# Performance work log

Hardware: AMD Instinct MI355X
Metric: run time of the kernel (lower is better)

The kernel has to match this reference:

```python
import jax, jax.numpy as jnp
import numpy as np

B, U, D, N, O = 128, 16, 256, 1024, 256
RES_CONN, IN_CONN, BIAS_P = 0.2, 0.2, 0.5


def _fixed_bernoulli(rng, heads, rows, cols, conn):
    # each column has exactly nb = int(conn*rows) ones (as in the torch code)
    nb = max(1, int(conn * rows))
    r = rng.random((heads, rows, cols))
    thr = np.sort(r, axis=1)[:, nb - 1:nb, :]
    return (r <= thr).astype(np.float32)


def setup_inputs() -> dict:
    rng = np.random.default_rng(0)
    # recurrent weights: normal * fixed-bernoulli mask, normalized by spectral radius
    W = rng.normal(size=(U, N, N)).astype(np.float32) * _fixed_bernoulli(rng, U, N, N, RES_CONN)
    sr0 = np.abs(np.linalg.eigvals(W.astype(np.float64))).max(axis=-1).astype(np.float32).reshape(U, 1, 1)
    W = W / sr0
    Win = _fixed_bernoulli(rng, U, D, N, IN_CONN)
    bias = (rng.random((U, 1, N)) < BIAS_P).astype(np.float32)
    Wout = rng.normal(size=(U, N, O)).astype(np.float32)
    adaptive_lr = rng.random((U, D, 1)).astype(np.float32)
    sr = rng.random((U, 1, 1)).astype(np.float32)
    temperature = np.ones((1,), np.float32)
    X = rng.normal(size=(B, U, D)).astype(np.float32)
    state = rng.normal(size=(B, U, N)).astype(np.float32)
    arrs = dict(X=X, state=state, W=W, Win=Win, bias=bias, Wout=Wout,
                sr=sr, adaptive_lr=adaptive_lr, temperature=temperature)
    return {k: jnp.asarray(v) for k, v in arrs.items()}


def reference(X, state, W, Win, bias, Wout, sr, adaptive_lr, temperature):
    # X: [B,U,D] -> [B,U,1,D]; state: [B,U,N] -> [B,U,1,N]
    x = X[:, :, None, :]
    s = state[:, :, None, :]
    # adaptive per-unit learning rate: softmax over the units axis
    lr = jax.nn.softmax(jnp.einsum('buid,udk->buik', x, adaptive_lr) / temperature, axis=1)  # [B,U,1,1]
    feed = jnp.einsum('buid,udn->buin', x, Win)            # [B,U,1,N]
    echo = jnp.einsum('buin,unm->buim', s, W * sr) + bias  # [B,U,1,N]
    new_state = (1.0 - lr) * s + lr * jnp.tanh(feed + echo)
    output = jnp.einsum('buin,uno->buio', new_state, Wout)  # [B,U,1,O]
    return new_state[:, :, 0, :], output[:, :, 0, :]
```

## Files before the change

### kernel.cpp

```cpp
#include <hip/hip_runtime.h>
#include <math.h>

#define Bsz 128
#define Usz 16
#define Dsz 256
#define Nsz 1024
#define Osz 256

typedef __attribute__((ext_vector_type(4))) float f32x4;
typedef __attribute__((ext_vector_type(8))) short bf16x8;

__device__ __forceinline__ unsigned short f2bf(float f) {
    union { float f; unsigned int u; } v; v.f = f;
    unsigned int lsb = (v.u >> 16) & 1u;
    v.u += 0x7fffu + lsb;
    return (unsigned short)(v.u >> 16);
}

__device__ __forceinline__ bf16x8 pack8(const float* x, float s) {
    union { bf16x8 v; unsigned short h[8]; } r;
    #pragma unroll
    for (int i = 0; i < 8; i++) r.h[i] = f2bf(x[i] * s);
    return r.v;
}

__global__ __launch_bounds__(256)
void lr_kernel(const float* __restrict__ X, const float* __restrict__ alr,
               const float* __restrict__ temp, float* __restrict__ lr)
{
    const int b = blockIdx.x;
    const int t = threadIdx.x;
    const int u = t >> 4;
    const int l = t & 15;
    const float* xp = X + ((size_t)b * Usz + u) * Dsz;
    const float* ap = alr + (size_t)u * Dsz;
    float s = 0.f;
    for (int d = l; d < Dsz; d += 16) s += xp[d] * ap[d];
    s += __shfl_down(s, 8, 16);
    s += __shfl_down(s, 4, 16);
    s += __shfl_down(s, 2, 16);
    s += __shfl_down(s, 1, 16);
    __shared__ float logits[16];
    if (l == 0) logits[u] = s;
    __syncthreads();
    if (t < 16) {
        const float T = temp[0];
        float m = -1e30f;
        #pragma unroll
        for (int i = 0; i < 16; i++) m = fmaxf(m, logits[i] / T);
        float sum = 0.f;
        #pragma unroll
        for (int i = 0; i < 16; i++) sum += expf(logits[i] / T - m);
        lr[(size_t)b * Usz + t] = expf(logits[t] / T - m) / sum;
    }
}

__global__ __launch_bounds__(256)
void state_mfma(const float* __restrict__ X, const float* __restrict__ state,
                const float* __restrict__ W, const float* __restrict__ Win,
                const float* __restrict__ bias, const float* __restrict__ sr,
                const float* __restrict__ lr, float* __restrict__ out0)
{
    const int id   = blockIdx.x;
    const int u    = id & 15;
    const int rest = id >> 4;
    const int nt   = rest & 15;
    const int mt   = rest >> 4;

    const int tid  = threadIdx.x;
    const int wave = tid >> 6, lane = tid & 63;
    const int l16  = lane & 15, kgl = lane >> 4;
    const int wrow = (wave & 1) * 16, wcol = (wave >> 1) * 32;

    __shared__ __align__(16) unsigned short As[2][1024];
    __shared__ __align__(16) unsigned short Bs[2][2048];

    f32x4 acc[2] = {};

    const int  sm  = tid & 31;
    const int  skg = (tid >> 5) & 3;
    const bool doA = tid < 128;
    const int  sb_n = tid & 63, sb_kg = tid >> 6;
    const float sru = sr[u];

    const float* Af = X     + ((size_t)(mt * 32 + sm) * Usz + u) * Dsz + skg * 8;
    const float* Ae = state + ((size_t)(mt * 32 + sm) * Usz + u) * Nsz + skg * 8;
    const float* Bf = Win + (size_t)u * Dsz * Nsz + (size_t)(sb_kg * 8) * Nsz + nt * 64 + sb_n;
    const float* Be = W   + (size_t)u * Nsz * Nsz + (size_t)(sb_kg * 8) * Nsz + nt * 64 + sb_n;

    float areg[8], breg[8];
    auto loadA = [&](int kb) {
        if (!doA) return;
        const float* p = (kb < Dsz) ? (Af + kb) : (Ae + (kb - Dsz));
        const f32x4 v0 = *(const f32x4*)p;
        const f32x4 v1 = *(const f32x4*)(p + 4);
        #pragma unroll
        for (int i = 0; i < 4; i++) { areg[i] = v0[i]; areg[4 + i] = v1[i]; }
    };
    auto loadB = [&](int kb) {
        const float* p = (kb < Dsz) ? (Bf + (size_t)kb * Nsz)
                                    : (Be + (size_t)(kb - Dsz) * Nsz);
        #pragma unroll
        for (int j = 0; j < 8; j++) breg[j] = p[(size_t)j * Nsz];
    };

    const int wrA = ((sm >> 4) * 4 + skg) * 128 + (sm & 15) * 8;
    const int wrB = ((sb_n >> 4) * 4 + sb_kg) * 128 + (sb_n & 15) * 8;
    auto writeBuf = [&](int buf, int kb) {
        const float asc = (kb < Dsz) ? 1.f : sru;
        if (doA) *(bf16x8*)&As[buf][wrA] = pack8(areg, asc);
        *(bf16x8*)&Bs[buf][wrB] = pack8(breg, 1.f);
    };

    loadA(0); loadB(0);
    writeBuf(0, 0);
    loadA(32); loadB(32);
    __syncthreads();

    const int aoff  = (((wave & 1) * 4 + kgl) * 16 + l16) * 8;
    const int boff0 = ((((wcol >> 4) + 0) * 4 + kgl) * 16 + l16) * 8;
    const int boff1 = ((((wcol >> 4) + 1) * 4 + kgl) * 16 + l16) * 8;

    for (int step = 0; step < 40; ++step) {
        const int buf = step & 1;
        if (step + 1 < 40) writeBuf(buf ^ 1, (step + 1) * 32);
        if (step + 2 < 40) { loadA((step + 2) * 32); loadB((step + 2) * 32); }
        const bf16x8 afr = *(const bf16x8*)&As[buf][aoff];
        const bf16x8 b0  = *(const bf16x8*)&Bs[buf][boff0];
        const bf16x8 b1  = *(const bf16x8*)&Bs[buf][boff1];
        acc[0] = __builtin_amdgcn_mfma_f32_16x16x32_bf16(afr, b0, acc[0], 0, 0, 0);
        acc[1] = __builtin_amdgcn_mfma_f32_16x16x32_bf16(afr, b1, acc[1], 0, 0, 0);
        __syncthreads();
    }

    #pragma unroll
    for (int ni = 0; ni < 2; ni++) {
        const int gcol = nt * 64 + wcol + ni * 16 + l16;
        const float bi = bias[u * Nsz + gcol];
        #pragma unroll
        for (int rg = 0; rg < 4; rg++) {
            const int grow = mt * 32 + wrow + kgl * 4 + rg;
            const size_t idx = ((size_t)grow * Usz + u) * Nsz + gcol;
            const float th = tanhf(acc[ni][rg] + bi);
            const float sv = state[idx];
            const float lv = lr[grow * Usz + u];
            out0[idx] = (1.f - lv) * sv + lv * th;
        }
    }
}

__global__ __launch_bounds__(256)
void out_mfma(const float* __restrict__ ns, const float* __restrict__ Wout,
              float* __restrict__ out1)
{
    const int id   = blockIdx.x;
    const int u    = id & 15;
    const int rest = id >> 4;
    const int ot   = rest & 3;
    const int mt   = rest >> 2;

    const int tid  = threadIdx.x;
    const int wave = tid >> 6, lane = tid & 63;
    const int l16  = lane & 15, kgl = lane >> 4;
    const int wcol = wave * 16;

    __shared__ __align__(16) unsigned short As[2][512];
    __shared__ __align__(16) unsigned short Bs[2][2048];

    f32x4 acc = {};

    const bool doA = tid < 64;
    const int  sm  = tid & 15, skg = (tid >> 4) & 3;
    const int  sb_n = tid & 63, sb_kg = tid >> 6;

    const float* Ap = ns + ((size_t)(mt * 16 + sm) * Usz + u) * Nsz + skg * 8;
    const float* Bp = Wout + (size_t)u * Nsz * Osz + (size_t)(sb_kg * 8) * Osz + ot * 64 + sb_n;

    float areg[8], breg[8];
    auto loadA = [&](int kb) {
        if (!doA) return;
        const f32x4 v0 = *(const f32x4*)(Ap + kb);
        const f32x4 v1 = *(const f32x4*)(Ap + kb + 4);
        #pragma unroll
        for (int i = 0; i < 4; i++) { areg[i] = v0[i]; areg[4 + i] = v1[i]; }
    };
    auto loadB = [&](int kb) {
        const float* p = Bp + (size_t)kb * Osz;
        #pragma unroll
        for (int j = 0; j < 8; j++) breg[j] = p[(size_t)j * Osz];
    };

    const int wrA = skg * 128 + sm * 8;
    const int wrB = ((sb_n >> 4) * 4 + sb_kg) * 128 + (sb_n & 15) * 8;
    auto writeBuf = [&](int buf) {
        if (doA) *(bf16x8*)&As[buf][wrA] = pack8(areg, 1.f);
        *(bf16x8*)&Bs[buf][wrB] = pack8(breg, 1.f);
    };

    loadA(0); loadB(0);
    writeBuf(0);
    loadA(32); loadB(32);
    __syncthreads();

    const int aoff = (kgl * 16 + l16) * 8;
    const int boff = ((wave * 4 + kgl) * 16 + l16) * 8;

    for (int step = 0; step < 32; ++step) {
        const int buf = step & 1;
        if (step + 1 < 32) writeBuf(buf ^ 1);
        if (step + 2 < 32) { loadA((step + 2) * 32); loadB((step + 2) * 32); }
        const bf16x8 afr = *(const bf16x8*)&As[buf][aoff];
        const bf16x8 bfr = *(const bf16x8*)&Bs[buf][boff];
        acc = __builtin_amdgcn_mfma_f32_16x16x32_bf16(afr, bfr, acc, 0, 0, 0);
        __syncthreads();
    }

    const int gcol = ot * 64 + wcol + l16;
    #pragma unroll
    for (int rg = 0; rg < 4; rg++) {
        const int grow = mt * 16 + kgl * 4 + rg;
        out1[((size_t)grow * Usz + u) * Osz + gcol] = acc[rg];
    }
}

extern "C" void kernel_launch(void* const* d_in, const int* in_sizes, int n_in,
                              void* d_out, int out_size, void* d_ws, size_t ws_size,
                              hipStream_t stream)
{
    (void)in_sizes; (void)n_in; (void)out_size; (void)ws_size;
    const float* X     = (const float*)d_in[0];
    const float* state = (const float*)d_in[1];
    const float* W     = (const float*)d_in[2];
    const float* Win   = (const float*)d_in[3];
    const float* bias  = (const float*)d_in[4];
    const float* Wout  = (const float*)d_in[5];
    const float* sr    = (const float*)d_in[6];
    const float* alr   = (const float*)d_in[7];
    const float* temp  = (const float*)d_in[8];

    float* out0 = (float*)d_out;
    float* out1 = out0 + (size_t)Bsz * Usz * Nsz;
    float* lr   = (float*)d_ws;

    lr_kernel<<<Bsz, 256, 0, stream>>>(X, alr, temp, lr);
    state_mfma<<<1024, 256, 0, stream>>>(X, state, W, Win, bias, sr, lr, out0);
    out_mfma<<<512, 256, 0, stream>>>(out0, Wout, out1);
}
```

Baseline: 203.8 us.

## Use full-batch M tiles, truncating bf16 packs, and split-K output GEMM

```diff
diff --git a/kernel.cpp b/kernel.cpp
--- a/kernel.cpp
+++ b/kernel.cpp
@@ -9,19 +9,21 @@
 
 typedef __attribute__((ext_vector_type(4))) float f32x4;
 typedef __attribute__((ext_vector_type(8))) short bf16x8;
-
-__device__ __forceinline__ unsigned short f2bf(float f) {
-    union { float f; unsigned int u; } v; v.f = f;
-    unsigned int lsb = (v.u >> 16) & 1u;
-    v.u += 0x7fffu + lsb;
-    return (unsigned short)(v.u >> 16);
-}
-
-__device__ __forceinline__ bf16x8 pack8(const float* x, float s) {
-    union { bf16x8 v; unsigned short h[8]; } r;
-    #pragma unroll
-    for (int i = 0; i < 8; i++) r.h[i] = f2bf(x[i] * s);
-    return r.v;
+typedef __attribute__((ext_vector_type(4))) unsigned int u32x4;
+
+union cell_u { u32x4 u; bf16x8 b; };
+
+__device__ __forceinline__ unsigned int fbits(float f) {
+    union { float f; unsigned int u; } v; v.f = f; return v.u;
+}
+__device__ __forceinline__ unsigned int pk(float lo, float hi) {
+    return __builtin_amdgcn_perm(fbits(hi), fbits(lo), 0x07060302u);
+}
+__device__ __forceinline__ u32x4 pk8(const float* x) {
+    u32x4 r;
+    r[0] = pk(x[0], x[1]); r[1] = pk(x[2], x[3]);
+    r[2] = pk(x[4], x[5]); r[3] = pk(x[6], x[7]);
+    return r;
 }
 
 __global__ __launch_bounds__(256)
@@ -61,55 +63,57 @@
                 const float* __restrict__ bias, const float* __restrict__ sr,
                 const float* __restrict__ lr, float* __restrict__ out0)
 {
-    const int id   = blockIdx.x;
-    const int u    = id & 15;
-    const int rest = id >> 4;
-    const int nt   = rest & 15;
-    const int mt   = rest >> 4;
+    const int id = blockIdx.x;
+    const int u  = id & 15;
+    const int nt = id >> 4;
 
     const int tid  = threadIdx.x;
     const int wave = tid >> 6, lane = tid & 63;
     const int l16  = lane & 15, kgl = lane >> 4;
-    const int wrow = (wave & 1) * 16, wcol = (wave >> 1) * 32;
-
-    __shared__ __align__(16) unsigned short As[2][1024];
-    __shared__ __align__(16) unsigned short Bs[2][2048];
-
-    f32x4 acc[2] = {};
-
-    const int  sm  = tid & 31;
-    const int  skg = (tid >> 5) & 3;
-    const bool doA = tid < 128;
-    const int  sb_n = tid & 63, sb_kg = tid >> 6;
+
+    __shared__ u32x4 As[2][512];
+    __shared__ u32x4 Bs[2][256];
+
+    f32x4 acc[8] = {};
+
+    const int am = tid & 127, akg2 = tid >> 7;
+    const int bn = tid & 63,  bkg  = tid >> 6;
     const float sru = sr[u];
 
-    const float* Af = X     + ((size_t)(mt * 32 + sm) * Usz + u) * Dsz + skg * 8;
-    const float* Ae = state + ((size_t)(mt * 32 + sm) * Usz + u) * Nsz + skg * 8;
-    const float* Bf = Win + (size_t)u * Dsz * Nsz + (size_t)(sb_kg * 8) * Nsz + nt * 64 + sb_n;
-    const float* Be = W   + (size_t)u * Nsz * Nsz + (size_t)(sb_kg * 8) * Nsz + nt * 64 + sb_n;
-
-    float areg[8], breg[8];
+    const float* Af = X     + ((size_t)am * Usz + u) * Dsz;
+    const float* Ae = state + ((size_t)am * Usz + u) * Nsz;
+    const float* Bf = Win + (size_t)u * Dsz * Nsz + nt * 64 + bn;
+    const float* Be = W   + (size_t)u * Nsz * Nsz + nt * 64 + bn;
+
+    float ar[16], br[8];
+
     auto loadA = [&](int kb) {
-        if (!doA) return;
-        const float* p = (kb < Dsz) ? (Af + kb) : (Ae + (kb - Dsz));
-        const f32x4 v0 = *(const f32x4*)p;
-        const f32x4 v1 = *(const f32x4*)(p + 4);
-        #pragma unroll
-        for (int i = 0; i < 4; i++) { areg[i] = v0[i]; areg[4 + i] = v1[i]; }
+        const int kk = kb + akg2 * 16;
+        const float* p = (kk < Dsz) ? (Af + kk) : (Ae + (kk - Dsz));
+        #pragma unroll
+        for (int q = 0; q < 4; q++) {
+            const f32x4 v = *(const f32x4*)(p + q * 4);
+            ar[q*4+0] = v[0]; ar[q*4+1] = v[1]; ar[q*4+2] = v[2]; ar[q*4+3] = v[3];
+        }
     };
     auto loadB = [&](int kb) {
-        const float* p = (kb < Dsz) ? (Bf + (size_t)kb * Nsz)
-                                    : (Be + (size_t)(kb - Dsz) * Nsz);
-        #pragma unroll
-        for (int j = 0; j < 8; j++) breg[j] = p[(size_t)j * Nsz];
-    };
-
-    const int wrA = ((sm >> 4) * 4 + skg) * 128 + (sm & 15) * 8;
-    const int wrB = ((sb_n >> 4) * 4 + sb_kg) * 128 + (sb_n & 15) * 8;
+        const int kk = kb + bkg * 8;
+        const float* p = (kk < Dsz) ? (Bf + (size_t)kk * Nsz)
+                                    : (Be + (size_t)(kk - Dsz) * Nsz);
+        #pragma unroll
+        for (int j = 0; j < 8; j++) br[j] = p[(size_t)j * Nsz];
+    };
+
+    const int ca = (am >> 4) * 64 + (akg2 * 2) * 16 + (am & 15);
+    const int cb = (bn >> 4) * 64 + bkg * 16 + (bn & 15);
     auto writeBuf = [&](int buf, int kb) {
-        const float asc = (kb < Dsz) ? 1.f : sru;
-        if (doA) *(bf16x8*)&As[buf][wrA] = pack8(areg, asc);
-        *(bf16x8*)&Bs[buf][wrB] = pack8(breg, 1.f);
+        As[buf][ca]      = pk8(ar);
+        As[buf][ca + 16] = pk8(ar + 8);
+        const float sc = (kb + bkg * 8 >= Dsz) ? sru : 1.f;
+        float t[8];
+        #pragma unroll
+        for (int j = 0; j < 8; j++) t[j] = br[j] * sc;
+        Bs[buf][cb] = pk8(t);
     };
 
     loadA(0); loadB(0);
@@ -117,31 +121,28 @@
     loadA(32); loadB(32);
     __syncthreads();
 
-    const int aoff  = (((wave & 1) * 4 + kgl) * 16 + l16) * 8;
-    const int boff0 = ((((wcol >> 4) + 0) * 4 + kgl) * 16 + l16) * 8;
-    const int boff1 = ((((wcol >> 4) + 1) * 4 + kgl) * 16 + l16) * 8;
-
     for (int step = 0; step < 40; ++step) {
         const int buf = step & 1;
         if (step + 1 < 40) writeBuf(buf ^ 1, (step + 1) * 32);
         if (step + 2 < 40) { loadA((step + 2) * 32); loadB((step + 2) * 32); }
-        const bf16x8 afr = *(const bf16x8*)&As[buf][aoff];
-        const bf16x8 b0  = *(const bf16x8*)&Bs[buf][boff0];
-        const bf16x8 b1  = *(const bf16x8*)&Bs[buf][boff1];
-        acc[0] = __builtin_amdgcn_mfma_f32_16x16x32_bf16(afr, b0, acc[0], 0, 0, 0);
-        acc[1] = __builtin_amdgcn_mfma_f32_16x16x32_bf16(afr, b1, acc[1], 0, 0, 0);
+        cell_u bc; bc.u = Bs[buf][wave * 64 + kgl * 16 + l16];
+        #pragma unroll
+        for (int mi = 0; mi < 8; mi++) {
+            cell_u ac; ac.u = As[buf][mi * 64 + kgl * 16 + l16];
+            acc[mi] = __builtin_amdgcn_mfma_f32_16x16x32_bf16(ac.b, bc.b, acc[mi], 0, 0, 0);
+        }
         __syncthreads();
     }
 
+    const int gcol = nt * 64 + wave * 16 + l16;
+    const float bi = bias[u * Nsz + gcol];
     #pragma unroll
-    for (int ni = 0; ni < 2; ni++) {
-        const int gcol = nt * 64 + wcol + ni * 16 + l16;
-        const float bi = bias[u * Nsz + gcol];
+    for (int mi = 0; mi < 8; mi++) {
         #pragma unroll
         for (int rg = 0; rg < 4; rg++) {
-            const int grow = mt * 32 + wrow + kgl * 4 + rg;
+            const int grow = mi * 16 + kgl * 4 + rg;
             const size_t idx = ((size_t)grow * Usz + u) * Nsz + gcol;
-            const float th = tanhf(acc[ni][rg] + bi);
+            const float th = tanhf(acc[mi][rg] + bi);
             const float sv = state[idx];
             const float lv = lr[grow * Usz + u];
             out0[idx] = (1.f - lv) * sv + lv * th;
@@ -151,50 +152,50 @@
 
 __global__ __launch_bounds__(256)
 void out_mfma(const float* __restrict__ ns, const float* __restrict__ Wout,
-              float* __restrict__ out1)
-{
-    const int id   = blockIdx.x;
-    const int u    = id & 15;
-    const int rest = id >> 4;
-    const int ot   = rest & 3;
-    const int mt   = rest >> 2;
+              float* __restrict__ dst, int nsteps, int partial)
+{
+    const int id = blockIdx.x;
+    const int u  = id & 15;
+    const int ot = id >> 4;
+    const int ks = blockIdx.y;
+    const int k0 = ks * nsteps * 32;
 
     const int tid  = threadIdx.x;
     const int wave = tid >> 6, lane = tid & 63;
     const int l16  = lane & 15, kgl = lane >> 4;
-    const int wcol = wave * 16;
-
-    __shared__ __align__(16) unsigned short As[2][512];
-    __shared__ __align__(16) unsigned short Bs[2][2048];
-
-    f32x4 acc = {};
-
-    const bool doA = tid < 64;
-    const int  sm  = tid & 15, skg = (tid >> 4) & 3;
-    const int  sb_n = tid & 63, sb_kg = tid >> 6;
-
-    const float* Ap = ns + ((size_t)(mt * 16 + sm) * Usz + u) * Nsz + skg * 8;
-    const float* Bp = Wout + (size_t)u * Nsz * Osz + (size_t)(sb_kg * 8) * Osz + ot * 64 + sb_n;
-
-    float areg[8], breg[8];
+
+    __shared__ u32x4 As[2][512];
+    __shared__ u32x4 Bs[2][256];
+
+    f32x4 acc[8] = {};
+
+    const int am = tid & 127, akg2 = tid >> 7;
+    const int bn = tid & 63,  bkg  = tid >> 6;
+
+    const float* Ap = ns + ((size_t)am * Usz + u) * Nsz + k0;
+    const float* Bp = Wout + (size_t)u * Nsz * Osz + (size_t)k0 * Osz + ot * 64 + bn;
+
+    float ar[16], br[8];
     auto loadA = [&](int kb) {
-        if (!doA) return;
-        const f32x4 v0 = *(const f32x4*)(Ap + kb);
-        const f32x4 v1 = *(const f32x4*)(Ap + kb + 4);
-        #pragma unroll
-        for (int i = 0; i < 4; i++) { areg[i] = v0[i]; areg[4 + i] = v1[i]; }
+        const float* p = Ap + kb + akg2 * 16;
+        #pragma unroll
+        for (int q = 0; q < 4; q++) {
+            const f32x4 v = *(const f32x4*)(p + q * 4);
+            ar[q*4+0] = v[0]; ar[q*4+1] = v[1]; ar[q*4+2] = v[2]; ar[q*4+3] = v[3];
+        }
     };
     auto loadB = [&](int kb) {
-        const float* p = Bp + (size_t)kb * Osz;
-        #pragma unroll
-        for (int j = 0; j < 8; j++) breg[j] = p[(size_t)j * Osz];
-    };
-
-    const int wrA = skg * 128 + sm * 8;
-    const int wrB = ((sb_n >> 4) * 4 + sb_kg) * 128 + (sb_n & 15) * 8;
+        const float* p = Bp + (size_t)(kb + bkg * 8) * Osz;
+        #pragma unroll
+        for (int j = 0; j < 8; j++) br[j] = p[(size_t)j * Osz];
+    };
+
+    const int ca = (am >> 4) * 64 + (akg2 * 2) * 16 + (am & 15);
+    const int cb = (bn >> 4) * 64 + bkg * 16 + (bn & 15);
     auto writeBuf = [&](int buf) {
-        if (doA) *(bf16x8*)&As[buf][wrA] = pack8(areg, 1.f);
-        *(bf16x8*)&Bs[buf][wrB] = pack8(breg, 1.f);
+        As[buf][ca]      = pk8(ar);
+        As[buf][ca + 16] = pk8(ar + 8);
+        Bs[buf][cb] = pk8(br);
     };
 
     loadA(0); loadB(0);
@@ -202,32 +203,56 @@
     loadA(32); loadB(32);
     __syncthreads();
 
-    const int aoff = (kgl * 16 + l16) * 8;
-    const int boff = ((wave * 4 + kgl) * 16 + l16) * 8;
-
-    for (int step = 0; step < 32; ++step) {
+    for (int step = 0; step < nsteps; ++step) {
         const int buf = step & 1;
-        if (step + 1 < 32) writeBuf(buf ^ 1);
-        if (step + 2 < 32) { loadA((step + 2) * 32); loadB((step + 2) * 32); }
-        const bf16x8 afr = *(const bf16x8*)&As[buf][aoff];
-        const bf16x8 bfr = *(const bf16x8*)&Bs[buf][boff];
-        acc = __builtin_amdgcn_mfma_f32_16x16x32_bf16(afr, bfr, acc, 0, 0, 0);
+        if (step + 1 < nsteps) writeBuf(buf ^ 1);
+        if (step + 2 < nsteps) { loadA((step + 2) * 32); loadB((step + 2) * 32); }
+        cell_u bc; bc.u = Bs[buf][wave * 64 + kgl * 16 + l16];
+        #pragma unroll
+        for (int mi = 0; mi < 8; mi++) {
+            cell_u ac; ac.u = As[buf][mi * 64 + kgl * 16 + l16];
+            acc[mi] = __builtin_amdgcn_mfma_f32_16x16x32_bf16(ac.b, bc.b, acc[mi], 0, 0, 0);
+        }
         __syncthreads();
     }
 
-    const int gcol = ot * 64 + wcol + l16;
+    const int c16 = wave * 16 + l16;
     #pragma unroll
-    for (int rg = 0; rg < 4; rg++) {
-        const int grow = mt * 16 + kgl * 4 + rg;
-        out1[((size_t)grow * Usz + u) * Osz + gcol] = acc[rg];
-    }
+    for (int mi = 0; mi < 8; mi++) {
+        #pragma unroll
+        for (int rg = 0; rg < 4; rg++) {
+            const int grow = mi * 16 + kgl * 4 + rg;
+            if (partial)
+                dst[((((size_t)ks * 16 + u) * 4 + ot) * 128 + grow) * 64 + c16] = acc[mi][rg];
+            else
+                dst[((size_t)grow * Usz + u) * Osz + ot * 64 + c16] = acc[mi][rg];
+        }
+    }
+}
+
+__global__ __launch_bounds__(256)
+void reduce_out(const float* __restrict__ part, float* __restrict__ out1)
+{
+    const int i = blockIdx.x * 256 + threadIdx.x;
+    const int base = i * 4;
+    const int m   = base >> 12;
+    const int u   = (base >> 8) & 15;
+    const int oc  = base & 255;
+    const int ot  = oc >> 6;
+    const int col = oc & 63;
+    const size_t pb = (((size_t)u * 4 + ot) * 128 + m) * 64 + col;
+    const size_t stride = (size_t)16 * 4 * 128 * 64;
+    f32x4 s = *(const f32x4*)(part + pb);
+    #pragma unroll
+    for (int ks = 1; ks < 4; ks++) s += *(const f32x4*)(part + pb + ks * stride);
+    *(f32x4*)(out1 + base) = s;
 }
 
 extern "C" void kernel_launch(void* const* d_in, const int* in_sizes, int n_in,
                               void* d_out, int out_size, void* d_ws, size_t ws_size,
                               hipStream_t stream)
 {
-    (void)in_sizes; (void)n_in; (void)out_size; (void)ws_size;
+    (void)in_sizes; (void)n_in; (void)out_size;
     const float* X     = (const float*)d_in[0];
     const float* state = (const float*)d_in[1];
     const float* W     = (const float*)d_in[2];
@@ -242,7 +267,17 @@
     float* out1 = out0 + (size_t)Bsz * Usz * Nsz;
     float* lr   = (float*)d_ws;
 
+    const size_t part_off = 8192;
+    const size_t part_bytes = (size_t)4 * 16 * 4 * 128 * 64 * 4;
+
     lr_kernel<<<Bsz, 256, 0, stream>>>(X, alr, temp, lr);
-    state_mfma<<<1024, 256, 0, stream>>>(X, state, W, Win, bias, sr, lr, out0);
-    out_mfma<<<512, 256, 0, stream>>>(out0, Wout, out1);
-}
+    state_mfma<<<256, 256, 0, stream>>>(X, state, W, Win, bias, sr, lr, out0);
+
+    if (ws_size >= part_off + part_bytes) {
+        float* part = (float*)((char*)d_ws + part_off);
+        out_mfma<<<dim3(64, 4), 256, 0, stream>>>(out0, Wout, part, 8, 1);
+        reduce_out<<<512, 256, 0, stream>>>(part, out1);
+    } else {
+        out_mfma<<<dim3(64, 1), 256, 0, stream>>>(out0, Wout, out1, 32, 0);
+    }
+}
```

New measurement: 195.8 us. -3.9%, faster.
